# Kernel optimization log

Measured on AMD Instinct MI355X. Metric: run time of the kernel, lower is better.

Reference implementation:

```python
import jax, jax.numpy as jnp
import numpy as np

B, H, W, N = 4, 64, 64, 64
NEAR, FAR = 2.0, 6.0
HID = 64


def setup_inputs() -> dict:
    key = jax.random.key(0)
    ks = jax.random.split(key, 6)
    ray_origins = jnp.tile(jnp.array([0.0, 0.0, 4.0], jnp.float32), (B, H, W, 1))
    ray_directions = jax.random.normal(ks[0], (B, H, W, 3), jnp.float32)
    tform_cam2world = jnp.eye(4, dtype=jnp.float32) + 0.1 * jax.random.normal(ks[1], (B, 4, 4), jnp.float32)
    depth_noise = jax.random.uniform(ks[2], (B, H, W, N), jnp.float32)
    u_samples = jax.random.uniform(ks[3], (B, H, W, N), jnp.float32)
    W1 = 0.5 * jax.random.normal(ks[4], (3, HID), jnp.float32)
    b1 = jnp.zeros((HID,), jnp.float32)
    W2 = 0.5 * jax.random.normal(ks[5], (HID, 4), jnp.float32)
    b2 = jnp.zeros((4,), jnp.float32)
    return dict(ray_origins=ray_origins, ray_directions=ray_directions,
                tform_cam2world=tform_cam2world, depth_noise=depth_noise,
                u_samples=u_samples, W1=W1, b1=b1, W2=W2, b2=b2)


def field(pts, W1, b1, W2, b2):
    # tiny radiance-field MLP standing in for the generator's sampler
    h = jax.nn.relu(pts @ W1 + b1)
    out = h @ W2 + b2
    sigma = out[..., 0]
    rgb = jax.nn.sigmoid(out[..., 1:4])
    return sigma, rgb


def compositing_weights(sigma, z_vals):
    # alpha-compositing weights (render_volume_density)
    dists = jnp.concatenate([z_vals[..., 1:] - z_vals[..., :-1],
                             jnp.full_like(z_vals[..., :1], 1e10)], axis=-1)
    alpha = 1.0 - jnp.exp(-jax.nn.relu(sigma) * dists)
    trans = jnp.cumprod(1.0 - alpha + 1e-10, axis=-1)
    trans = jnp.concatenate([jnp.ones_like(trans[..., :1]), trans[..., :-1]], axis=-1)
    return alpha * trans


def sample_pdf(bins, weights, u):
    # bins [R, M+1], weights [R, M], u [R, S] -> samples [R, S]
    pdf = weights / jnp.sum(weights, axis=-1, keepdims=True)
    cdf = jnp.cumsum(pdf, axis=-1)
    cdf = jnp.concatenate([jnp.zeros_like(cdf[..., :1]), cdf], axis=-1)  # [R, M+1]
    inds = jax.vmap(lambda c, uu: jnp.searchsorted(c, uu, side='right'))(cdf, u)
    last = cdf.shape[-1] - 1
    below = jnp.clip(inds - 1, 0, last)
    above = jnp.clip(inds, 0, last)
    cdf_b = jnp.take_along_axis(cdf, below, axis=-1)
    cdf_a = jnp.take_along_axis(cdf, above, axis=-1)
    bin_b = jnp.take_along_axis(bins, below, axis=-1)
    bin_a = jnp.take_along_axis(bins, above, axis=-1)
    denom = cdf_a - cdf_b
    denom = jnp.where(denom < 1e-5, 1.0, denom)
    t = (u - cdf_b) / denom
    return bin_b + t * (bin_a - bin_b)


def reference(ray_origins, ray_directions, tform_cam2world, depth_noise, u_samples, W1, b1, W2, b2):
    rd = ray_directions / jnp.linalg.norm(ray_directions, axis=-1, keepdims=True)
    # stratified coarse samples along each ray
    t = (jnp.arange(N, dtype=jnp.float32) + depth_noise) / N           # [B,H,W,N]
    z_vals = NEAR + (FAR - NEAR) * t
    pts = ray_origins[..., None, :] + rd[..., None, :] * z_vals[..., None]
    sigma, rgb = field(pts, W1, b1, W2, b2)                            # [B,H,W,N], [B,H,W,N,3]

    # --- hierarchical importance sampling (no_grad in original) ---
    w = compositing_weights(sigma, z_vals).reshape(-1, N)              # [R,N]
    pad = jnp.pad(w, ((0, 0), (1, 1)), constant_values=-jnp.inf)
    mx = jnp.maximum(pad[:, :-1], pad[:, 1:])                          # max_pool1d(k=2,s=1,p=1) -> [R,N+1]
    sm = 0.5 * (mx[:, :-1] + mx[:, 1:]) + 0.01                        # avg_pool1d(k=2,s=1)  -> [R,N]
    z_mid = (0.5 * (z_vals[..., 1:] + z_vals[..., :-1])).reshape(-1, N - 1)
    z_samples = sample_pdf(z_mid, sm[:, 1:-1], u_samples.reshape(-1, N))
    z_samples = jax.lax.stop_gradient(z_samples.reshape(B, H, W, N))

    # fine evaluation + merge-sort of coarse/fine samples
    z_all = jnp.concatenate([z_vals, z_samples], axis=-1)              # [B,H,W,2N]
    idx = jnp.argsort(z_all, axis=-1)
    z_sorted = jnp.take_along_axis(z_all, idx, axis=-1)
    pts_f = ray_origins[..., None, :] + rd[..., None, :] * z_samples[..., None]
    sigma_f, rgb_f = field(pts_f, W1, b1, W2, b2)
    sigma_all = jnp.take_along_axis(jnp.concatenate([sigma, sigma_f], axis=-1), idx, axis=-1)
    rgb_cat = jnp.concatenate([rgb, rgb_f], axis=-2)
    rgb_all = jnp.take_along_axis(rgb_cat, jnp.broadcast_to(idx[..., None], idx.shape + (3,)), axis=-2)

    # final alpha compositing
    w_all = compositing_weights(sigma_all, z_sorted)
    rgb_pred = jnp.sum(w_all[..., None] * rgb_all, axis=-2)            # [B,H,W,3]
    depth_pred = jnp.sum(w_all * z_sorted, axis=-1)                    # [B,H,W]
    mask_pred = jnp.sum(w_all, axis=-1)                                # [B,H,W]

    # camera-space depth (invert_space: R_w2c = R^T)
    R_w2c = jnp.swapaxes(tform_cam2world[:, :3, :3], -1, -2)           # [B,3,3]
    view_dir = jnp.einsum('bhwj,bij->bhwi', rd, R_w2c)
    depth_cam = -(view_dir * depth_pred[..., None])[..., -1]
    return rgb_pred, depth_cam, mask_pred
```

## Files before the change

kernel.cpp:

```cpp
#include <hip/hip_runtime.h>
#include <hip/hip_bf16.h>
#include <math.h>

#define Nn    64
#define RPB   4
#define NRAYS 16384
#define NEARV 2.0f
#define FARV  6.0f

typedef __attribute__((ext_vector_type(8))) short bf16x8;
typedef __attribute__((ext_vector_type(4))) float f32x4;
typedef __attribute__((ext_vector_type(2))) float f32x2;

template <int CTRL, int RMASK>
__device__ __forceinline__ float dpp_mv(float x, float ident) {
  return __int_as_float(__builtin_amdgcn_update_dpp(
      __float_as_int(ident), __float_as_int(x), CTRL, RMASK, 0xf, false));
}
__device__ __forceinline__ float shfl_up1(float x) {
  return __int_as_float(__builtin_amdgcn_update_dpp(
      __float_as_int(x), __float_as_int(x), 0x138, 0xf, 0xf, false));
}
__device__ __forceinline__ float shfl_dn1(float x) {
  return __int_as_float(__builtin_amdgcn_update_dpp(
      __float_as_int(x), __float_as_int(x), 0x130, 0xf, 0xf, false));
}
__device__ __forceinline__ float scan_add_dpp(float x) {
  x += dpp_mv<0x111, 0xf>(x, 0.f);
  x += dpp_mv<0x112, 0xf>(x, 0.f);
  x += dpp_mv<0x114, 0xf>(x, 0.f);
  x += dpp_mv<0x118, 0xf>(x, 0.f);
  x += dpp_mv<0x142, 0xa>(x, 0.f);
  x += dpp_mv<0x143, 0xc>(x, 0.f);
  return x;
}
__device__ __forceinline__ float scan_mul_dpp(float x) {
  x *= dpp_mv<0x111, 0xf>(x, 1.f);
  x *= dpp_mv<0x112, 0xf>(x, 1.f);
  x *= dpp_mv<0x114, 0xf>(x, 1.f);
  x *= dpp_mv<0x118, 0xf>(x, 1.f);
  x *= dpp_mv<0x142, 0xa>(x, 1.f);
  x *= dpp_mv<0x143, 0xc>(x, 1.f);
  return x;
}
__device__ __forceinline__ float reduce_add_bcast(float x) {
  x = scan_add_dpp(x);
  return __int_as_float(__builtin_amdgcn_readlane(__float_as_int(x), 63));
}

__device__ __forceinline__ float fast_rcp(float x) { return __builtin_amdgcn_rcpf(x); }
__device__ __forceinline__ float sigmoidf_fast(float x) { return fast_rcp(1.f + __expf(-x)); }

__device__ __forceinline__ short bfhi_bits(float x) { return (short)(__float_as_uint(x) >> 16); }
__device__ __forceinline__ float bfhi_val(float x)  { return __uint_as_float(__float_as_uint(x) & 0xFFFF0000u); }

template <int LEVEL, int D>
__device__ __forceinline__ void bitonic_stage(unsigned& k, int lane) {
  unsigned t;
  if constexpr (D == 32) {
    t = (unsigned)__builtin_amdgcn_ds_bpermute((lane ^ 32) << 2, (int)k);
  } else {
    t = (unsigned)__builtin_amdgcn_ds_swizzle((int)k, (D << 10) | 0x1F);
  }
  const bool bitd = (lane & D) != 0;
  const bool desc = (lane & (1 << LEVEL)) != 0;
  const unsigned mn = (k < t) ? k : t;
  const unsigned mx = (k < t) ? t : k;
  k = (bitd == desc) ? mn : mx;
}
template <int LEVEL, int D>
struct BSort {
  static __device__ __forceinline__ void run(unsigned& k, int lane) {
    bitonic_stage<LEVEL, D>(k, lane);
    if constexpr (D > 1) BSort<LEVEL, D / 2>::run(k, lane);
    else if constexpr (LEVEL < 6) BSort<LEVEL + 1, (1 << LEVEL)>::run(k, lane);
  }
};

__device__ __forceinline__ int count_lt_key(unsigned arr, unsigned x) {
  int cnt = 0;
#pragma unroll
  for (int step = 64; step >= 1; step >>= 1) {
    const int idx = cnt + step - 1;
    const unsigned v = (unsigned)__shfl((int)arr, idx, 64);
    if (idx < 64 && v < x) cnt += step;
  }
  return cnt;
}
__device__ __forceinline__ int count_le_f(float arr, float x) {
  int cnt = 0;
#pragma unroll
  for (int step = 64; step >= 1; step >>= 1) {
    const int idx = cnt + step - 1;
    const float v = __shfl(arr, idx, 64);
    if (idx < 63 && v <= x) cnt += step;
  }
  return cnt;
}

template <bool SPLITB>
__device__ __forceinline__ void field_eval(
    float zlane, const f32x2 c0v[2][4], const f32x2 c1v[2][4],
    const bf16x8 aHi[2], const bf16x8 aLo[2],
    float b20, float b21, float b22, float b23,
    int quad, int col, float4* scratch, float o[4]) {
#pragma unroll
  for (int nt = 0; nt < 4; ++nt) {
    f32x4 acc = {0.f, 0.f, 0.f, 0.f};
    const float zm = __shfl(zlane, nt * 16 + col, 64);
    const f32x2 zm2 = {zm, zm};
#pragma unroll
    for (int ks = 0; ks < 2; ++ks) {
      union { bf16x8 v; unsigned u[4]; } Bhi, Blo;
#pragma unroll
      for (int p = 0; p < 4; ++p) {
        f32x2 h = zm2 * c1v[ks][p] + c0v[ks][p];
        h = __builtin_elementwise_max(h, (f32x2){0.f, 0.f});
        if constexpr (SPLITB) {
          union { f32x2 f; unsigned u[2]; } U; U.f = h;
          Bhi.u[p] = __builtin_amdgcn_perm(U.u[1], U.u[0], 0x07060302u);
          union { unsigned u[2]; f32x2 f; } M;
          M.u[0] = U.u[0] & 0xFFFF0000u;
          M.u[1] = U.u[1] & 0xFFFF0000u;
          const f32x2 l = h - M.f;
          union { f32x2 f; unsigned u[2]; } L; L.f = l;
          Blo.u[p] = __builtin_amdgcn_perm(L.u[1], L.u[0], 0x07060302u);
        } else {
          __hip_bfloat162 t = __float22bfloat162_rn(make_float2(h[0], h[1]));
          Bhi.u[p] = *reinterpret_cast<unsigned*>(&t);
        }
      }
      if constexpr (SPLITB) {
        acc = __builtin_amdgcn_mfma_f32_16x16x32_bf16(aHi[ks], Bhi.v, acc, 0, 0, 0);
        acc = __builtin_amdgcn_mfma_f32_16x16x32_bf16(aHi[ks], Blo.v, acc, 0, 0, 0);
        acc = __builtin_amdgcn_mfma_f32_16x16x32_bf16(aLo[ks], Bhi.v, acc, 0, 0, 0);
      } else {
        acc = __builtin_amdgcn_mfma_f32_16x16x32_bf16(aHi[ks], Bhi.v, acc, 0, 0, 0);
        acc = __builtin_amdgcn_mfma_f32_16x16x32_bf16(aLo[ks], Bhi.v, acc, 0, 0, 0);
      }
    }
    if (quad == 0) scratch[nt * 16 + col] = make_float4(acc[0], acc[1], acc[2], acc[3]);
  }
  const float4 r = scratch[(threadIdx.x & 63)];
  o[0] = r.x + b20; o[1] = r.y + b21; o[2] = r.z + b22; o[3] = r.w + b23;
}

__global__ __launch_bounds__(RPB * 64, 4) void nerf_fused(
    const float* __restrict__ ray_o, const float* __restrict__ ray_d,
    const float* __restrict__ tform, const float* __restrict__ noise,
    const float* __restrict__ usmp,  const float* __restrict__ W1,
    const float* __restrict__ b1,    const float* __restrict__ W2,
    const float* __restrict__ b2,    float* __restrict__ out) {
  const int wave = threadIdx.x >> 6;
  const int lane = threadIdx.x & 63;
  const int ray  = blockIdx.x * RPB + wave;
  const int quad = lane >> 4;
  const int col  = lane & 15;

  __shared__ float2 sC [RPB][Nn];
  __shared__ float  sZs[RPB][2 * Nn];
  __shared__ float4 sPk[RPB][2 * Nn];

  const float o0 = ray_o[ray * 3 + 0], o1 = ray_o[ray * 3 + 1], o2 = ray_o[ray * 3 + 2];
  float d0 = ray_d[ray * 3 + 0], d1 = ray_d[ray * 3 + 1], d2 = ray_d[ray * 3 + 2];
  const float rn = __builtin_amdgcn_rsqf(d0 * d0 + d1 * d1 + d2 * d2);
  d0 *= rn; d1 *= rn; d2 *= rn;

  {
    const float w10 = W1[lane], w11 = W1[64 + lane], w12 = W1[128 + lane];
    const float c1 = d0 * w10 + d1 * w11 + d2 * w12;
    const float c0 = o0 * w10 + o1 * w11 + o2 * w12 + b1[lane];
    sC[wave][lane] = make_float2(c0, c1);
  }

  const float nz = noise[ray * Nn + lane];
  const float z  = NEARV + (FARV - NEARV) * ((float)lane + nz) * (1.0f / Nn);
  const unsigned kc = ((__float_as_uint(z) - 0x40000000u) << 7) | (unsigned)lane;

  f32x2 c0v[2][4], c1v[2][4];
#pragma unroll
  for (int ks = 0; ks < 2; ++ks) {
    const float4* cc4 = (const float4*)&sC[wave][0];
    const int base4 = (ks * 32 + quad * 8) >> 1;
#pragma unroll
    for (int jj = 0; jj < 4; ++jj) {
      const float4 v = cc4[base4 + jj];
      c0v[ks][jj] = (f32x2){v.x, v.z};
      c1v[ks][jj] = (f32x2){v.y, v.w};
    }
  }

  bf16x8 aHi[2], aLo[2];
#pragma unroll
  for (int ks = 0; ks < 2; ++ks) {
#pragma unroll
    for (int j = 0; j < 8; ++j) {
      const int k = ks * 32 + quad * 8 + j;
      const float wv  = (col < 4) ? W2[k * 4 + col] : 0.f;
      aHi[ks][j] = bfhi_bits(wv);
      aLo[ks][j] = bfhi_bits(wv - bfhi_val(wv));
    }
  }
  const float b20 = b2[0], b21 = b2[1], b22 = b2[2], b23 = b2[3];
  float4* scratch = &sPk[wave][0];

  float oc[4];
  field_eval<true>(z, c0v, c1v, aHi, aLo, b20, b21, b22, b23, quad, col, scratch, oc);
  const float sig = oc[0];
  const float cr = sigmoidf_fast(oc[1]), cg = sigmoidf_fast(oc[2]), cb = sigmoidf_fast(oc[3]);

  const float zn   = shfl_dn1(z);
  const float dist = (lane == 63) ? 1e10f : (zn - z);
  const float alpha = 1.f - __expf(-fmaxf(sig, 0.f) * dist);
  float cdfreg, binreg;
  {
    const float P  = scan_mul_dpp(1.f - alpha + 1e-10f);
    float Te = shfl_up1(P);
    if (lane == 0) Te = 1.f;
    const float w = alpha * Te;

    const float mxA = fmaxf(shfl_up1(w), w);
    const float mxB = fmaxf(w, shfl_dn1(w));
    const float sm = 0.5f * (mxA + mxB) + 0.01f;

    const float v   = (lane >= 1 && lane <= 62) ? sm : 0.f;
    const float tot = reduce_add_bcast(v);
    const float pdf = v * fast_rcp(tot);
    const float C   = scan_add_dpp(pdf);
    cdfreg = (lane == 0) ? 0.f : C;
    binreg = 0.5f * (z + zn);
  }

  const float u = usmp[ray * Nn + lane];
  const int lo = count_le_f(cdfreg, u);
  const int below = lo - 1;
  const int above = (lo < 63) ? lo : 62;
  const float cdfb = __shfl(cdfreg, below, 64);
  const float cdfa = __shfl(cdfreg, above, 64);
  const float binb = __shfl(binreg, below, 64);
  const float bina = __shfl(binreg, above, 64);
  float den = cdfa - cdfb;
  if (den < 1e-5f) den = 1.f;
  const float zs = fmaf((u - cdfb) * fast_rcp(den), bina - binb, binb);

  float of[4];
  field_eval<false>(zs, c0v, c1v, aHi, aLo, b20, b21, b22, b23, quad, col, scratch, of);
  const float sigF = of[0];
  const float fr = sigmoidf_fast(of[1]), fg = sigmoidf_fast(of[2]), fb = sigmoidf_fast(of[3]);

  const unsigned kf = ((__float_as_uint(zs) - 0x40000000u) << 7) | (unsigned)(64 + lane);

  unsigned kfS = kf;
  BSort<1, 1>::run(kfS, lane);
  const int r1 = __builtin_amdgcn_ds_permute((int)((kfS & 63u) << 2), lane);

  const int lo1 = count_lt_key(kc, kf);
  const int lo2 = count_lt_key(kfS, kc);
  const int p0 = lane + lo2;
  const int p1 = r1 + lo1;

  sZs[wave][p0] = z;
  sZs[wave][p1] = zs;
  sPk[wave][p0] = make_float4(sig,  cr, cg, cb);
  sPk[wave][p1] = make_float4(sigF, fr, fg, fb);

  const float2 zz = *(const float2*)&sZs[wave][2 * lane];
  const float z0 = zz.x, z1 = zz.y;
  const float z2 = shfl_dn1(z0);
  const float dist0 = z1 - z0;
  const float dist1 = (lane == 63) ? 1e10f : (z2 - z1);
  const float4 q0 = sPk[wave][2 * lane];
  const float4 q1 = sPk[wave][2 * lane + 1];
  const float al0 = 1.f - __expf(-fmaxf(q0.x, 0.f) * dist0);
  const float al1 = 1.f - __expf(-fmaxf(q1.x, 0.f) * dist1);
  const float aa0 = 1.f - al0 + 1e-10f;
  const float aa1 = 1.f - al1 + 1e-10f;
  const float Pp = scan_mul_dpp(aa0 * aa1);
  float Tp = shfl_up1(Pp);
  if (lane == 0) Tp = 1.f;
  const float w0 = al0 * Tp;
  const float w1 = al1 * Tp * aa0;

  const float accR = reduce_add_bcast(w0 * q0.y + w1 * q1.y);
  const float accG = reduce_add_bcast(w0 * q0.z + w1 * q1.z);
  const float accB = reduce_add_bcast(w0 * q0.w + w1 * q1.w);
  const float accD = reduce_add_bcast(w0 * z0 + w1 * z1);
  const float accM = reduce_add_bcast(w0 + w1);

  if (lane == 0) {
    const float* tf = tform + (ray >> 12) * 16;
    const float vz = d0 * tf[2] + d1 * tf[6] + d2 * tf[10];
    out[ray * 3 + 0]     = accR;
    out[ray * 3 + 1]     = accG;
    out[ray * 3 + 2]     = accB;
    out[NRAYS * 3 + ray] = -vz * accD;
    out[NRAYS * 4 + ray] = accM;
  }
}

extern "C" void kernel_launch(void* const* d_in, const int* in_sizes, int n_in,
                              void* d_out, int out_size, void* d_ws, size_t ws_size,
                              hipStream_t stream) {
  const float* ray_o = (const float*)d_in[0];
  const float* ray_d = (const float*)d_in[1];
  const float* tform = (const float*)d_in[2];
  const float* noise = (const float*)d_in[3];
  const float* usmp  = (const float*)d_in[4];
  const float* W1    = (const float*)d_in[5];
  const float* b1    = (const float*)d_in[6];
  const float* W2    = (const float*)d_in[7];
  const float* b2    = (const float*)d_in[8];
  float* out = (float*)d_out;

  nerf_fused<<<dim3(NRAYS / RPB), RPB * 64, 0, stream>>>(
      ray_o, ray_d, tform, noise, usmp, W1, b1, W2, b2, out);
}
```

Baseline: 104.4 us.

## Replace rank-based merge with bitonic merge network and key-decoded gather

Replaces the two binary-search rank computations (count_lt_key, each doing seven dependent shuffles) and the scatter into shared memory with a bitonic merge of the coarse keys and the reversed sorted fine keys, split into low and high halves. Sorted z values are decoded straight from the keys, and the per-sample sigma/rgb records are gathered from shared memory using the index bits embedded in each key. This drops the sZs array and the scatter step but adds more cross-lane swizzle and bpermute operations. The intent is to shorten the serial dependency chain in the merge.

Result: faster. 102.2 us (-2.2%).

```diff
diff --git a/kernel.cpp b/kernel.cpp
--- a/kernel.cpp
+++ b/kernel.cpp
@@ -77,16 +77,27 @@
   }
 };
 
-__device__ __forceinline__ int count_lt_key(unsigned arr, unsigned x) {
-  int cnt = 0;
-#pragma unroll
-  for (int step = 64; step >= 1; step >>= 1) {
-    const int idx = cnt + step - 1;
-    const unsigned v = (unsigned)__shfl((int)arr, idx, 64);
-    if (idx < 64 && v < x) cnt += step;
-  }
-  return cnt;
-}
+template <int D>
+__device__ __forceinline__ void merge_stage(unsigned& k, int lane) {
+  unsigned t;
+  if constexpr (D == 32) {
+    t = (unsigned)__builtin_amdgcn_ds_bpermute((lane ^ 32) << 2, (int)k);
+  } else {
+    t = (unsigned)__builtin_amdgcn_ds_swizzle((int)k, (D << 10) | 0x1F);
+  }
+  const unsigned mn = (k < t) ? k : t;
+  const unsigned mx = (k < t) ? t : k;
+  k = ((lane & D) != 0) ? mx : mn;
+}
+__device__ __forceinline__ void merge64(unsigned& k, int lane) {
+  merge_stage<32>(k, lane);
+  merge_stage<16>(k, lane);
+  merge_stage<8>(k, lane);
+  merge_stage<4>(k, lane);
+  merge_stage<2>(k, lane);
+  merge_stage<1>(k, lane);
+}
+
 __device__ __forceinline__ int count_le_f(float arr, float x) {
   int cnt = 0;
 #pragma unroll
@@ -158,7 +169,6 @@
   const int col  = lane & 15;
 
   __shared__ float2 sC [RPB][Nn];
-  __shared__ float  sZs[RPB][2 * Nn];
   __shared__ float4 sPk[RPB][2 * Nn];
 
   const float o0 = ray_o[ray * 3 + 0], o1 = ray_o[ray * 3 + 1], o2 = ray_o[ray * 3 + 2];
@@ -202,12 +212,13 @@
     }
   }
   const float b20 = b2[0], b21 = b2[1], b22 = b2[2], b23 = b2[3];
-  float4* scratch = &sPk[wave][0];
+  float4* scratch = &sPk[wave][64];
 
   float oc[4];
   field_eval<true>(z, c0v, c1v, aHi, aLo, b20, b21, b22, b23, quad, col, scratch, oc);
   const float sig = oc[0];
   const float cr = sigmoidf_fast(oc[1]), cg = sigmoidf_fast(oc[2]), cb = sigmoidf_fast(oc[3]);
+  sPk[wave][lane] = make_float4(sig, cr, cg, cb);
 
   const float zn   = shfl_dn1(z);
   const float dist = (lane == 63) ? 1e10f : (zn - z);
@@ -232,9 +243,9 @@
   }
 
   const float u = usmp[ray * Nn + lane];
-  const int lo = count_le_f(cdfreg, u);
-  const int below = lo - 1;
-  const int above = (lo < 63) ? lo : 62;
+  const int lo_i = count_le_f(cdfreg, u);
+  const int below = lo_i - 1;
+  const int above = (lo_i < 63) ? lo_i : 62;
   const float cdfb = __shfl(cdfreg, below, 64);
   const float cdfa = __shfl(cdfreg, above, 64);
   const float binb = __shfl(binreg, below, 64);
@@ -247,30 +258,40 @@
   field_eval<false>(zs, c0v, c1v, aHi, aLo, b20, b21, b22, b23, quad, col, scratch, of);
   const float sigF = of[0];
   const float fr = sigmoidf_fast(of[1]), fg = sigmoidf_fast(of[2]), fb = sigmoidf_fast(of[3]);
+  sPk[wave][64 + lane] = make_float4(sigF, fr, fg, fb);
 
   const unsigned kf = ((__float_as_uint(zs) - 0x40000000u) << 7) | (unsigned)(64 + lane);
 
   unsigned kfS = kf;
   BSort<1, 1>::run(kfS, lane);
-  const int r1 = __builtin_amdgcn_ds_permute((int)((kfS & 63u) << 2), lane);
-
-  const int lo1 = count_lt_key(kc, kf);
-  const int lo2 = count_lt_key(kfS, kc);
-  const int p0 = lane + lo2;
-  const int p1 = r1 + lo1;
-
-  sZs[wave][p0] = z;
-  sZs[wave][p1] = zs;
-  sPk[wave][p0] = make_float4(sig,  cr, cg, cb);
-  sPk[wave][p1] = make_float4(sigF, fr, fg, fb);
-
-  const float2 zz = *(const float2*)&sZs[wave][2 * lane];
-  const float z0 = zz.x, z1 = zz.y;
+
+  unsigned lok = kc;
+  unsigned hik = (unsigned)__builtin_amdgcn_ds_bpermute((63 - lane) << 2, (int)kfS);
+  {
+    const unsigned mn = (lok < hik) ? lok : hik;
+    const unsigned mx = (lok < hik) ? hik : lok;
+    lok = mn; hik = mx;
+  }
+  merge64(lok, lane);
+  merge64(hik, lane);
+
+  const int a0 = ((2 * lane) & 63) << 2;
+  const int a1 = ((2 * lane + 1) & 63) << 2;
+  const unsigned l0 = (unsigned)__builtin_amdgcn_ds_bpermute(a0, (int)lok);
+  const unsigned h0 = (unsigned)__builtin_amdgcn_ds_bpermute(a0, (int)hik);
+  const unsigned l1 = (unsigned)__builtin_amdgcn_ds_bpermute(a1, (int)lok);
+  const unsigned h1 = (unsigned)__builtin_amdgcn_ds_bpermute(a1, (int)hik);
+  const unsigned k0 = (lane < 32) ? l0 : h0;
+  const unsigned k1 = (lane < 32) ? l1 : h1;
+
+  const float z0 = __uint_as_float((k0 >> 7) + 0x40000000u);
+  const float z1 = __uint_as_float((k1 >> 7) + 0x40000000u);
+  const float4 q0 = sPk[wave][k0 & 127u];
+  const float4 q1 = sPk[wave][k1 & 127u];
+
   const float z2 = shfl_dn1(z0);
   const float dist0 = z1 - z0;
   const float dist1 = (lane == 63) ? 1e10f : (z2 - z1);
-  const float4 q0 = sPk[wave][2 * lane];
-  const float4 q1 = sPk[wave][2 * lane + 1];
   const float al0 = 1.f - __expf(-fmaxf(q0.x, 0.f) * dist0);
   const float al1 = 1.f - __expf(-fmaxf(q1.x, 0.f) * dist1);
   const float aa0 = 1.f - al0 + 1e-10f;
```
